# Optimization experiments

Hardware: AMD Instinct MI355X
Metric: run time of the kernel (lower is better)

The kernel has to match this reference:

```python
import jax, jax.numpy as jnp
import numpy as np

EPS = 1e-6
K_MEM, C_MEM = 512, 2048
SEQ, BATCH = 256, 16
NUM_LAYERS, NUM_HEADS, HEAD_DIM = 12, 12, 64
KV_DIM = NUM_LAYERS * NUM_HEADS * HEAD_DIM * 2  # 18432
NOISE_STD = 0.01
PINV_STEPS = 3
BEN_COHEN_INIT = -5.0


def approx_pinv(A, steps=PINV_STEPS):
    # Ben-Cohen iterative pseudoinverse. A: (B, M, N) -> (B, N, M)
    alpha = jnp.minimum(jnp.exp(jnp.float32(BEN_COHEN_INIT)), jnp.float32(5e-4))  # clamp(max=5e-4)
    P = alpha * jnp.swapaxes(A, -2, -1)
    for _ in range(steps):
        P = 2.0 * P - (P @ A) @ P  # matches bmm(bmm(P, A), P)
    return P


def setup_inputs() -> dict:
    key = jax.random.key(0)
    ks = jax.random.split(key, 6)
    lim = np.sqrt(6.0 / (C_MEM + KV_DIM))  # xavier_uniform
    return {
        "z_sequence": jax.random.normal(ks[0], (SEQ, BATCH, C_MEM), jnp.float32),
        "z_query": jax.random.normal(ks[1], (BATCH, C_MEM), jnp.float32),
        "noise": jax.random.normal(ks[2], (SEQ, BATCH, C_MEM), jnp.float32),
        "memory_mean": jax.random.normal(ks[3], (K_MEM, C_MEM), jnp.float32) * 0.02,
        "memory_logvar": jnp.zeros((K_MEM,), jnp.float32),
        "w_logvar": jnp.zeros((1,), jnp.float32),
        "W_M_weight": jax.random.uniform(ks[4], (KV_DIM, C_MEM), jnp.float32, -lim, lim),
    }


def reference(z_sequence, z_query, noise, memory_mean, memory_logvar, w_logvar, W_M_weight):
    B = z_query.shape[0]
    # ---- write ----
    prior_var = jnp.exp(memory_logvar) + EPS                     # (K,)
    prior_mean_b = jnp.broadcast_to(memory_mean, (B, K_MEM, C_MEM))
    z_noise = z_sequence + noise * NOISE_STD                     # (S, B, C)
    z_t = jnp.swapaxes(z_noise, 0, 1)                            # (B, S, C)
    M_pinv = approx_pinv(prior_mean_b)                           # (B, C, K)
    w = z_t @ M_pinv                                             # (B, S, K)
    w_pinv = approx_pinv(w)                                      # (B, K, S)
    new_memory_mean = w_pinv @ z_t                               # (B, K, C)
    # KL divergence (post_var == prior_var here)
    t1 = C_MEM * jnp.sum(prior_var / prior_var)
    t2 = jnp.sum((new_memory_mean - prior_mean_b) ** 2 / prior_var[None, :, None], axis=(-2, -1))
    t3 = -jnp.float32(C_MEM * K_MEM)
    t4 = C_MEM * jnp.sum(jnp.log(prior_var) - jnp.log(prior_var))
    dkl_M = jnp.mean(t1 + t2 + t3 + t4)
    # ---- read (deterministic addressing) ----
    M_pinv2 = approx_pinv(new_memory_mean)                       # (B, C, K)
    w_mean = jnp.einsum('bc,bck->bk', z_query, M_pinv2)          # (B, K)
    z_retrieved = jnp.einsum('bk,bkc->bc', w_mean, new_memory_mean)  # (B, C)
    Z_r_kv = z_retrieved @ W_M_weight.T                          # (B, kv_dim)
    wl = jnp.broadcast_to(w_logvar, w_mean.shape)
    dkl_w = 0.5 * jnp.sum(jnp.exp(wl) + w_mean ** 2 - 1.0 - wl)
    return z_retrieved, Z_r_kv, dkl_M, dkl_w
```

## Files before the change

### kernel.cpp

```cpp
#include <hip/hip_runtime.h>

#define ALPHA 5.0e-4f

typedef short s16x8 __attribute__((ext_vector_type(8)));
typedef unsigned short u16x8 __attribute__((ext_vector_type(8)));
typedef unsigned short u16x4 __attribute__((ext_vector_type(4)));
typedef float f32x4 __attribute__((ext_vector_type(4)));

__device__ __forceinline__ unsigned short f2bf(float f) {
    unsigned int u = __builtin_bit_cast(unsigned int, f);
    u += 0x7fffu + ((u >> 16) & 1u);
    return (unsigned short)(u >> 16);
}
__device__ __forceinline__ float bf2f(unsigned short h) {
    return __builtin_bit_cast(float, (unsigned int)h << 16);
}
__device__ __forceinline__ f32x4 mfma16(s16x8 a, s16x8 b, f32x4 c) {
    return __builtin_amdgcn_mfma_f32_16x16x32_bf16(a, b, c, 0, 0, 0);
}

template<int ROWS>
__device__ __forceinline__ void stage_kcontig(const float* __restrict__ src, int ld,
                                              unsigned short* __restrict__ lds, int tid)
{
#pragma unroll
    for (int it = 0; it < ROWS * 8 / 256; ++it) {
        const int g = tid + it * 256;
        const int row = g >> 3, s = g & 7;
        const float* p = src + (long long)row * ld + s * 8;
        const float4 x0 = *(const float4*)p;
        const float4 x1 = *(const float4*)(p + 4);
        u16x8 h;
        h[0] = f2bf(x0.x); h[1] = f2bf(x0.y); h[2] = f2bf(x0.z); h[3] = f2bf(x0.w);
        h[4] = f2bf(x1.x); h[5] = f2bf(x1.y); h[6] = f2bf(x1.z); h[7] = f2bf(x1.w);
        *(u16x8*)(lds + row * 64 + ((s ^ (row & 7)) << 3)) = h;
    }
}

template<int ROWS>
__device__ __forceinline__ void stage_kstrided(const float* __restrict__ src, int ld,
                                               unsigned short* __restrict__ lds, int tid)
{
    constexpr int KPT = ROWS * 64 / 256;
    const int m = tid % ROWS, kb = (tid / ROWS) * KPT;
#pragma unroll
    for (int j8 = 0; j8 < KPT / 8; ++j8) {
        u16x8 h;
#pragma unroll
        for (int j = 0; j < 8; ++j)
            h[j] = f2bf(src[(long long)(kb + j8 * 8 + j) * ld + m]);
        const int s = (kb >> 3) + j8;
        *(u16x8*)(lds + m * 64 + ((s ^ (m & 7)) << 3)) = h;
    }
}

template<int ROWS>
__device__ __forceinline__ void stage_kcontig_b(const unsigned short* __restrict__ src, int ld,
                                                unsigned short* __restrict__ lds, int tid)
{
#pragma unroll
    for (int it = 0; it < ROWS * 8 / 256; ++it) {
        const int g = tid + it * 256;
        const int row = g >> 3, s = g & 7;
        const u16x8 h = *(const u16x8*)(src + (long long)row * ld + s * 8);
        *(u16x8*)(lds + row * 64 + ((s ^ (row & 7)) << 3)) = h;
    }
}

template<int ROWS>
__device__ __forceinline__ void stage_kstrided_b(const unsigned short* __restrict__ src, int ld,
                                                 unsigned short* __restrict__ lds, int tid)
{
    constexpr int KPT = ROWS * 64 / 256;
    const int m = tid % ROWS, kb = (tid / ROWS) * KPT;
#pragma unroll
    for (int j8 = 0; j8 < KPT / 8; ++j8) {
        u16x8 h;
#pragma unroll
        for (int j = 0; j < 8; ++j)
            h[j] = src[(long long)(kb + j8 * 8 + j) * ld + m];
        const int s = (kb >> 3) + j8;
        *(u16x8*)(lds + m * 64 + ((s ^ (m & 7)) << 3)) = h;
    }
}

template<int BM, int BN, bool TA, bool TB>
__device__ __forceinline__
void gemm_dev_f32(int bx, int by,
                  const float* __restrict__ A, int lda,
                  const float* __restrict__ B, int ldb,
                  float* __restrict__ D, int ldd, int Kd)
{
    constexpr int TWM = BM / 2, TWN = BN / 2;
    constexpr int FM = TWM / 16, FN = TWN / 16;
    __shared__ unsigned short As[BM * 64];
    __shared__ unsigned short Bs[BN * 64];

    const int tid = threadIdx.x;
    const int lane = tid & 63, w = tid >> 6;
    const int wm = w >> 1, wn = w & 1;
    const int lrow = lane & 15, lk = lane >> 4;
    const int m0 = by * BM, n0 = bx * BN;

    f32x4 acc[FM][FN];
#pragma unroll
    for (int i = 0; i < FM; ++i)
#pragma unroll
        for (int j = 0; j < FN; ++j) acc[i][j] = (f32x4){0.f, 0.f, 0.f, 0.f};

    for (int k0 = 0; k0 < Kd; k0 += 64) {
        if (!TA) stage_kcontig<BM>(A + (long long)m0 * lda + k0, lda, As, tid);
        else     stage_kstrided<BM>(A + (long long)k0 * lda + m0, lda, As, tid);
        if (TB)  stage_kcontig<BN>(B + (long long)n0 * ldb + k0, ldb, Bs, tid);
        else     stage_kstrided<BN>(B + (long long)k0 * ldb + n0, ldb, Bs, tid);
        __syncthreads();
#pragma unroll
        for (int kk = 0; kk < 2; ++kk) {
            s16x8 ah[FM], bh[FN];
#pragma unroll
            for (int i = 0; i < FM; ++i) {
                const int row = wm * TWM + i * 16 + lrow;
                const int s = kk * 4 + lk;
                ah[i] = *(const s16x8*)(As + row * 64 + ((s ^ (row & 7)) << 3));
            }
#pragma unroll
            for (int j = 0; j < FN; ++j) {
                const int col = wn * TWN + j * 16 + lrow;
                const int s = kk * 4 + lk;
                bh[j] = *(const s16x8*)(Bs + col * 64 + ((s ^ (col & 7)) << 3));
            }
#pragma unroll
            for (int i = 0; i < FM; ++i)
#pragma unroll
                for (int j = 0; j < FN; ++j)
                    acc[i][j] = mfma16(ah[i], bh[j], acc[i][j]);
        }
        __syncthreads();
    }

#pragma unroll
    for (int i = 0; i < FM; ++i)
#pragma unroll
        for (int j = 0; j < FN; ++j) {
            const int col = n0 + wn * TWN + j * 16 + lrow;
#pragma unroll
            for (int r = 0; r < 4; ++r) {
                const int row = m0 + wm * TWM + i * 16 + lk * 4 + r;
                D[(long long)row * ldd + col] = acc[i][j][r];
            }
        }
}

__global__ __launch_bounds__(256)
void fused_prep_kernel(const float* __restrict__ zs, const float* __restrict__ no,
                       const float* __restrict__ zq, const float* __restrict__ mm,
                       unsigned short* __restrict__ ztb, float* __restrict__ q,
                       float* __restrict__ Gp)
{
    const int blk = blockIdx.x, t = threadIdx.x;
    if (blk % 9 == 8) {
        const int g = blk / 9;
        const int ky = g & 7;
        const int tile = g >> 3;
        gemm_dev_f32<64, 64, false, true>(
            tile & 7, tile >> 3,
            mm + ky * 256, 2048, mm + ky * 256, 2048,
            Gp + (long long)ky * 262144, 512, 256);
    } else {
        const int bs = blk - blk / 9;
        const int b = bs >> 8, sI = bs & 255;
        const long long in = ((long long)sI * 16 + b) * 2048 + t * 8;
        const f32x4 z0 = __builtin_nontemporal_load((const f32x4*)(zs + in));
        const f32x4 z1 = __builtin_nontemporal_load((const f32x4*)(zs + in + 4));
        const f32x4 n0 = __builtin_nontemporal_load((const f32x4*)(no + in));
        const f32x4 n1 = __builtin_nontemporal_load((const f32x4*)(no + in + 4));
        float zf[8];
#pragma unroll
        for (int j = 0; j < 4; ++j) {
            zf[j]     = fmaf(0.01f, n0[j], z0[j]);
            zf[j + 4] = fmaf(0.01f, n1[j], z1[j]);
        }
        u16x8 o;
#pragma unroll
        for (int j = 0; j < 8; ++j) o[j] = f2bf(zf[j]);
        *(u16x8*)(ztb + ((long long)bs * 2048 + t * 8)) = o;
        const float4 q0 = *(const float4*)(zq + b * 2048 + t * 8);
        const float4 q1 = *(const float4*)(zq + b * 2048 + t * 8 + 4);
        float qa = zf[0] * q0.x + zf[1] * q0.y + zf[2] * q0.z + zf[3] * q0.w
                 + zf[4] * q1.x + zf[5] * q1.y + zf[6] * q1.z + zf[7] * q1.w;
        __shared__ float red[256];
        red[t] = qa; __syncthreads();
        for (int st = 128; st > 0; st >>= 1) { if (t < st) red[t] += red[t + st]; __syncthreads(); }
        if (t == 0) q[bs] = red[0];
    }
}

__global__ __launch_bounds__(256)
void g1_reduce_zero_kernel(const float* __restrict__ Gp,
                           unsigned short* __restrict__ G1b,
                           float* __restrict__ wmean, float* __restrict__ out)
{
    const int blk = blockIdx.x, tid = threadIdx.x;
    if (blk < 256) {
        const int idx = blk * 256 + tid;
        f32x4 s = {0.f, 0.f, 0.f, 0.f};
#pragma unroll
        for (int p = 0; p < 8; ++p) {
            const f32x4 v = *(const f32x4*)(Gp + (long long)p * 262144 + idx * 4);
            s[0] += v[0]; s[1] += v[1]; s[2] += v[2]; s[3] += v[3];
        }
        u16x4 h;
#pragma unroll
        for (int j = 0; j < 4; ++j) h[j] = f2bf(s[j]);
        *(u16x4*)(G1b + idx * 4) = h;
    } else {
        const int zb = blk - 256;
        float4* oz = (float4*)(out + 32768);
        const int base = (zb * 256 + tid) * 32;
#pragma unroll
        for (int i = 0; i < 32; ++i) oz[base + i] = (float4){0.f, 0.f, 0.f, 0.f};
        if (zb == 0) {
            float4* wm4 = (float4*)wmean;
            for (int i = tid; i < 2048; i += 256) wm4[i] = (float4){0.f, 0.f, 0.f, 0.f};
            if (tid == 0) out[327680] = 0.f;
        }
    }
}

__global__ __launch_bounds__(256)
void p1_kernel(const float* __restrict__ mm, const unsigned short* __restrict__ G1b,
               unsigned short* __restrict__ P1b)
{
    constexpr int BM = 64, BN = 64, TWM = 32, TWN = 32, FM = 2, FN = 2;
    __shared__ unsigned short As[BM * 64];
    __shared__ unsigned short Bs[BN * 64];
    const int blk = blockIdx.x;
    const int bx = blk & 7, by = blk >> 3;
    const int tid = threadIdx.x;
    const int lane = tid & 63, w = tid >> 6;
    const int wm = w >> 1, wn = w & 1;
    const int lrow = lane & 15, lk = lane >> 4;
    const int m0 = by * BM, n0 = bx * BN;

    f32x4 acc[FM][FN];
#pragma unroll
    for (int i = 0; i < FM; ++i)
#pragma unroll
        for (int j = 0; j < FN; ++j) acc[i][j] = (f32x4){0.f, 0.f, 0.f, 0.f};

    for (int k0 = 0; k0 < 512; k0 += 64) {
        stage_kstrided<BM>(mm + (long long)k0 * 2048 + m0, 2048, As, tid);
        stage_kstrided_b<BN>(G1b + (long long)k0 * 512 + n0, 512, Bs, tid);
        __syncthreads();
#pragma unroll
        for (int kk = 0; kk < 2; ++kk) {
            s16x8 ah[FM], bh[FN];
#pragma unroll
            for (int i = 0; i < FM; ++i) {
                const int row = wm * TWM + i * 16 + lrow;
                const int s = kk * 4 + lk;
                ah[i] = *(const s16x8*)(As + row * 64 + ((s ^ (row & 7)) << 3));
            }
#pragma unroll
            for (int j = 0; j < FN; ++j) {
                const int col = wn * TWN + j * 16 + lrow;
                const int s = kk * 4 + lk;
                bh[j] = *(const s16x8*)(Bs + col * 64 + ((s ^ (col & 7)) << 3));
            }
#pragma unroll
            for (int i = 0; i < FM; ++i)
#pragma unroll
                for (int j = 0; j < FN; ++j)
                    acc[i][j] = mfma16(ah[i], bh[j], acc[i][j]);
        }
        __syncthreads();
    }

    const float al = -28.0f * ALPHA * ALPHA, be = 8.0f * ALPHA;
#pragma unroll
    for (int i = 0; i < FM; ++i)
#pragma unroll
        for (int j = 0; j < FN; ++j) {
            const int col = n0 + wn * TWN + j * 16 + lrow;
#pragma unroll
            for (int r = 0; r < 4; ++r) {
                const int row = m0 + wm * TWM + i * 16 + lk * 4 + r;
                const float v = fmaf(be, mm[(long long)col * 2048 + row], al * acc[i][j][r]);
                P1b[(long long)row * 512 + col] = f2bf(v);
            }
        }
}

__global__ __launch_bounds__(256)
void wT_u_kernel(const unsigned short* __restrict__ ztb,
                 const unsigned short* __restrict__ P1b,
                 unsigned short* __restrict__ wTb,
                 const float* __restrict__ q, float* __restrict__ wmean)
{
    constexpr int BM = 64, BN = 64, TWM = 32, TWN = 32, FM = 2, FN = 2;
    __shared__ unsigned short As[BM * 64];
    __shared__ unsigned short Bs[BN * 64];
    const int lin = blockIdx.x;
    const int r = lin & 7, t = lin >> 3;
    const int by = r + 8 * (t & 7), bx = t >> 3;
    const int tid = threadIdx.x;
    const int lane = tid & 63, w = tid >> 6;
    const int wm = w >> 1, wn = w & 1;
    const int lrow = lane & 15, lk = lane >> 4;
    const int m0 = by * BM, n0 = bx * BN;

    f32x4 acc[FM][FN];
#pragma unroll
    for (int i = 0; i < FM; ++i)
#pragma unroll
        for (int j = 0; j < FN; ++j) acc[i][j] = (f32x4){0.f, 0.f, 0.f, 0.f};

    for (int k0 = 0; k0 < 2048; k0 += 64) {
        stage_kcontig_b<BM>(ztb + (long long)m0 * 2048 + k0, 2048, As, tid);
        stage_kstrided_b<BN>(P1b + (long long)k0 * 512 + n0, 512, Bs, tid);
        __syncthreads();
#pragma unroll
        for (int kk = 0; kk < 2; ++kk) {
            s16x8 ah[FM], bh[FN];
#pragma unroll
            for (int i = 0; i < FM; ++i) {
                const int row = wm * TWM + i * 16 + lrow;
                const int s = kk * 4 + lk;
                ah[i] = *(const s16x8*)(As + row * 64 + ((s ^ (row & 7)) << 3));
            }
#pragma unroll
            for (int j = 0; j < FN; ++j) {
                const int col = wn * TWN + j * 16 + lrow;
                const int s = kk * 4 + lk;
                bh[j] = *(const s16x8*)(Bs + col * 64 + ((s ^ (col & 7)) << 3));
            }
#pragma unroll
            for (int i = 0; i < FM; ++i)
#pragma unroll
                for (int j = 0; j < FN; ++j)
                    acc[i][j] = mfma16(ah[i], bh[j], acc[i][j]);
        }
        __syncthreads();
    }

    float up[FN] = {0.f, 0.f};
#pragma unroll
    for (int i = 0; i < FM; ++i)
#pragma unroll
        for (int rr = 0; rr < 4; ++rr) {
            const int row = m0 + wm * TWM + i * 16 + lk * 4 + rr;
            const float qv = q[row];
#pragma unroll
            for (int j = 0; j < FN; ++j) {
                const int col = n0 + wn * TWN + j * 16 + lrow;
                const float v = acc[i][j][rr];
                wTb[(long long)(row >> 8) * 131072 + (long long)col * 256 + (row & 255)] = f2bf(v);
                up[j] = fmaf(v, qv, up[j]);
            }
        }
    const int b = m0 >> 8;
#pragma unroll
    for (int j = 0; j < FN; ++j) {
        float v = up[j];
        v += __shfl_xor(v, 16);
        v += __shfl_xor(v, 32);
        if (lk == 0) {
            const int col = n0 + wn * TWN + j * 16 + lrow;
            atomicAdd(&wmean[b * 512 + col], (64.0f * ALPHA * ALPHA) * v);
        }
    }
}

__global__ __launch_bounds__(256)
void tail1_kernel(const unsigned short* __restrict__ wTb,
                  const unsigned short* __restrict__ ztb,
                  const float* __restrict__ wmean, const float* __restrict__ wlv,
                  float* __restrict__ out)
{
    __shared__ __align__(16) float smemf[1024];
    const int blk = blockIdx.x, tid = threadIdx.x;
    if (blk < 256) {
        float* wms = smemf;
        float* ys  = smemf + 512;
        float* red2 = smemf + 768;
        const int r8 = blk & 7, t8 = blk >> 3;
        const int b = r8 + 8 * (t8 & 1), ct = t8 >> 1;
        wms[tid] = wmean[b * 512 + tid];
        wms[tid + 256] = wmean[b * 512 + 256 + tid];
        __syncthreads();
        {
            const unsigned short* wp = wTb + (long long)b * 131072 + tid;
            float yv = 0.f;
#pragma unroll 8
            for (int k = 0; k < 512; ++k)
                yv = fmaf(wms[k], bf2f(wp[(long long)k * 256]), yv);
            ys[tid] = yv;
        }
        __syncthreads();
        const int c = ct * 128 + (tid & 127), sh = tid >> 7;
        const unsigned short* zp = ztb + (long long)b * 524288 + c;
        float acc2 = 0.f;
        const int sbase = sh * 128;
#pragma unroll 8
        for (int s = 0; s < 128; ++s)
            acc2 = fmaf(ys[sbase + s], bf2f(zp[(long long)(sbase + s) * 2048]), acc2);
        red2[tid] = acc2; __syncthreads();
        if (sh == 0)
            out[(long long)b * 2048 + c] = (8.0f * ALPHA) * (red2[tid] + red2[tid + 128]);
    } else {
        float* red = smemf;
        float s = 0.f;
        for (int i = tid; i < 16 * 512; i += 256) { const float v = wmean[i]; s += v * v; }
        red[tid] = s; __syncthreads();
        for (int st = 128; st > 0; st >>= 1) { if (tid < st) red[tid] += red[tid + st]; __syncthreads(); }
        if (tid == 0) {
            const float l = wlv[0];
            out[327681] = 0.5f * (red[0] + 8192.0f * (expf(l) - 1.0f - l));
        }
    }
}

__global__ __launch_bounds__(256)
void tail2_kernel(const unsigned short* __restrict__ wTb,
                  const unsigned short* __restrict__ ztb,
                  const float* __restrict__ mm, const float* __restrict__ mlv,
                  const float* __restrict__ WM, float* __restrict__ out)
{
    __shared__ __align__(16) unsigned char smem[34304];
    const int g = blockIdx.x, tid = threadIdx.x;
    const int grp = g / 26, p = g % 26;
    if (p < 8) {
        constexpr int BM = 128, BN = 128, TWM = 64, TWN = 64, FM = 4, FN = 4;
        unsigned short* As = (unsigned short*)smem;
        unsigned short* Bs = As + BM * 64;
        float* ivars = (float*)(smem + 32768);
        float* red = (float*)(smem + 33280);
        const int bz = ((2 * grp + p) & 7) + 8 * (grp & 1);
        const int rest = grp >> 1;
        const int by = rest & 3, bx = rest >> 2;
        const int lane = tid & 63, w = tid >> 6;
        const int wm = w >> 1, wn = w & 1;
        const int lrow = lane & 15, lk = lane >> 4;
        const int m0 = by * BM, n0 = bx * BN;

        if (tid < 128) ivars[tid] = 1.0f / (expf(mlv[m0 + tid]) + 1e-6f);

        f32x4 acc[FM][FN];
#pragma unroll
        for (int i = 0; i < FM; ++i)
#pragma unroll
            for (int j = 0; j < FN; ++j) acc[i][j] = (f32x4){0.f, 0.f, 0.f, 0.f};

        for (int k0 = 0; k0 < 256; k0 += 64) {
            stage_kcontig_b<BM>(wTb + (long long)bz * 131072 + (long long)m0 * 256 + k0, 256, As, tid);
            stage_kstrided_b<BN>(ztb + (long long)bz * 524288 + (long long)k0 * 2048 + n0, 2048, Bs, tid);
            __syncthreads();
#pragma unroll
            for (int kk = 0; kk < 2; ++kk) {
                s16x8 ah[FM], bh[FN];
#pragma unroll
                for (int i = 0; i < FM; ++i) {
                    const int row = wm * TWM + i * 16 + lrow;
                    const int s = kk * 4 + lk;
                    ah[i] = *(const s16x8*)(As + row * 64 + ((s ^ (row & 7)) << 3));
                }
#pragma unroll
                for (int j = 0; j < FN; ++j) {
                    const int col = wn * TWN + j * 16 + lrow;
                    const int s = kk * 4 + lk;
                    bh[j] = *(const s16x8*)(Bs + col * 64 + ((s ^ (col & 7)) << 3));
                }
#pragma unroll
                for (int i = 0; i < FM; ++i)
#pragma unroll
                    for (int j = 0; j < FN; ++j)
                        acc[i][j] = mfma16(ah[i], bh[j], acc[i][j]);
            }
            __syncthreads();
        }

        const float A8 = 8.0f * ALPHA;
        float da = 0.f;
#pragma unroll
        for (int i = 0; i < FM; ++i)
#pragma unroll
            for (int j = 0; j < FN; ++j) {
                const int cl = wn * TWN + j * 16 + lrow;
#pragma unroll
                for (int rr = 0; rr < 4; ++rr) {
                    const int rl = wm * TWM + i * 16 + lk * 4 + rr;
                    const float v = A8 * acc[i][j][rr];
                    const float d = v - mm[(long long)(m0 + rl) * 2048 + (n0 + cl)];
                    da = fmaf(d * d, ivars[rl], da);
                }
            }
        red[tid] = da; __syncthreads();
        for (int st = 128; st > 0; st >>= 1) { if (tid < st) red[tid] += red[tid + st]; __syncthreads(); }
        if (tid == 0) atomicAdd(&out[327680], red[0] * (1.0f / 16.0f));
    } else {
        const int z = grp * 18 + (p - 8);
        const int bx = z % 288, ky = z / 288;
        const int lane = tid & 63, w = tid >> 6;
        const int d0 = bx * 64 + w * 16;
        const int kc0 = ky * 256;
        const int rr = lane & 15, kq = lane >> 4;
        const float* zr = out;
        s16x8 areg[8];
        const float* zb = zr + rr * 2048 + kc0 + kq * 8;
#pragma unroll
        for (int s = 0; s < 8; ++s) {
            const f32x4 a0 = *(const f32x4*)(zb + s * 32);
            const f32x4 a1 = *(const f32x4*)(zb + s * 32 + 4);
            u16x8 h;
#pragma unroll
            for (int j = 0; j < 4; ++j) { h[j] = f2bf(a0[j]); h[j + 4] = f2bf(a1[j]); }
            areg[s] = __builtin_bit_cast(s16x8, h);
        }
        f32x4 acc = {0.f, 0.f, 0.f, 0.f};
        const float* wb = WM + (long long)(d0 + rr) * 2048 + kc0 + kq * 8;
#pragma unroll
        for (int s = 0; s < 8; ++s) {
            const f32x4 b0 = __builtin_nontemporal_load((const f32x4*)(wb + s * 32));
            const f32x4 b1 = __builtin_nontemporal_load((const f32x4*)(wb + s * 32 + 4));
            u16x8 h;
#pragma unroll
            for (int j = 0; j < 4; ++j) { h[j] = f2bf(b0[j]); h[j + 4] = f2bf(b1[j]); }
            acc = mfma16(areg[s], __builtin_bit_cast(s16x8, h), acc);
        }
        float* oz = out + 32768;
#pragma unroll
        for (int r = 0; r < 4; ++r)
            atomicAdd(&oz[(long long)(kq * 4 + r) * 18432 + d0 + rr], acc[r]);
    }
}

extern "C" void kernel_launch(void* const* d_in, const int* in_sizes, int n_in,
                              void* d_out, int out_size, void* d_ws, size_t ws_size,
                              hipStream_t stream)
{
    (void)in_sizes; (void)n_in; (void)out_size; (void)ws_size;
    const float* z_seq   = (const float*)d_in[0];
    const float* z_query = (const float*)d_in[1];
    const float* noise   = (const float*)d_in[2];
    const float* mm      = (const float*)d_in[3];
    const float* mlv     = (const float*)d_in[4];
    const float* wlv     = (const float*)d_in[5];
    const float* WM      = (const float*)d_in[6];
    float* out = (float*)d_out;

    char* wsb = (char*)d_ws;
    unsigned short* ztb  = (unsigned short*)(wsb);
    unsigned short* wTb  = (unsigned short*)(wsb + (16LL << 20));
    float*          Gp   = (float*)(wsb + (24LL << 20));
    unsigned short* G1b  = (unsigned short*)(wsb + (32LL << 20));
    unsigned short* P1b  = (unsigned short*)(wsb + (33LL << 20));
    float*          qvec = (float*)(wsb + (36LL << 20));
    float*          wmean = (float*)(wsb + (37LL << 20));

    fused_prep_kernel<<<4608, 256, 0, stream>>>(z_seq, noise, z_query, mm,
                                                ztb, qvec, Gp);
    g1_reduce_zero_kernel<<<265, 256, 0, stream>>>(Gp, G1b, wmean, out);
    p1_kernel<<<256, 256, 0, stream>>>(mm, G1b, P1b);
    wT_u_kernel<<<512, 256, 0, stream>>>(ztb, P1b, wTb, qvec, wmean);
    tail1_kernel<<<257, 256, 0, stream>>>(wTb, ztb, wmean, wlv, out);
    tail2_kernel<<<3328, 256, 0, stream>>>(wTb, ztb, mm, mlv, WM, out);
}
```

Before: 164.0 us.

## Reassociate P1 product into Z·M^T then G1, fuse with reduce, prefetch W_M

Reorders the matrix chain: instead of forming P1 = 8αM^T - 28α²M^T G1 and then multiplying by Z (K=2048), it computes V = Z·M^T (K=2048) in the same launch as the G1 reduction. A second GEMM with K=512 then forms w = 8αV - 28α² V·G1. This drops a kernel launch and the dependency of the large GEMM on G1. Extra idle blocks in vg_kernel and tail1 read chunks of W_M so it is warm in the last-level cache for tail2, which now uses plain loads instead of nontemporal ones. The trade-offs are additional bandwidth spent on prefetch and rounding V to bf16 before the second product.

```diff
diff --git a/kernel.cpp b/kernel.cpp
--- a/kernel.cpp
+++ b/kernel.cpp
@@ -17,6 +17,19 @@
 }
 __device__ __forceinline__ f32x4 mfma16(s16x8 a, s16x8 b, f32x4 c) {
     return __builtin_amdgcn_mfma_f32_16x16x32_bf16(a, b, c, 0, 0, 0);
+}
+
+__device__ __forceinline__ void prefetch_chunk(const float* __restrict__ WM,
+                                               int chunk, int tid)
+{
+    const float4* wp = (const float4*)WM + (long long)chunk * 12288;
+    float4 s = {0.f, 0.f, 0.f, 0.f};
+#pragma unroll 8
+    for (int i = 0; i < 48; ++i) {
+        const float4 v = wp[tid + i * 256];
+        s.x += v.x; s.y += v.y; s.z += v.z; s.w += v.w;
+    }
+    asm volatile("" :: "v"(s.x), "v"(s.y), "v"(s.z), "v"(s.w));
 }
 
 template<int ROWS>
@@ -196,13 +209,70 @@
 }
 
 __global__ __launch_bounds__(256)
-void g1_reduce_zero_kernel(const float* __restrict__ Gp,
-                           unsigned short* __restrict__ G1b,
-                           float* __restrict__ wmean, float* __restrict__ out)
+void vg_kernel(const unsigned short* __restrict__ ztb, const float* __restrict__ mm,
+               const float* __restrict__ Gp, const float* __restrict__ WM,
+               unsigned short* __restrict__ Vb, unsigned short* __restrict__ G1b,
+               float* __restrict__ wmean, float* __restrict__ out)
 {
     const int blk = blockIdx.x, tid = threadIdx.x;
-    if (blk < 256) {
-        const int idx = blk * 256 + tid;
+    if (blk < 512) {
+        constexpr int BM = 64, BN = 64, TWM = 32, TWN = 32, FM = 2, FN = 2;
+        __shared__ unsigned short As[BM * 64];
+        __shared__ unsigned short Bs[BN * 64];
+        const int r = blk & 7, t = blk >> 3;
+        const int by = r + 8 * (t & 7), bx = t >> 3;
+        const int lane = tid & 63, w = tid >> 6;
+        const int wm = w >> 1, wn = w & 1;
+        const int lrow = lane & 15, lk = lane >> 4;
+        const int m0 = by * BM, n0 = bx * BN;
+
+        f32x4 acc[FM][FN];
+#pragma unroll
+        for (int i = 0; i < FM; ++i)
+#pragma unroll
+            for (int j = 0; j < FN; ++j) acc[i][j] = (f32x4){0.f, 0.f, 0.f, 0.f};
+
+        for (int k0 = 0; k0 < 2048; k0 += 64) {
+            stage_kcontig_b<BM>(ztb + (long long)m0 * 2048 + k0, 2048, As, tid);
+            stage_kcontig<BN>(mm + (long long)n0 * 2048 + k0, 2048, Bs, tid);
+            __syncthreads();
+#pragma unroll
+            for (int kk = 0; kk < 2; ++kk) {
+                s16x8 ah[FM], bh[FN];
+#pragma unroll
+                for (int i = 0; i < FM; ++i) {
+                    const int row = wm * TWM + i * 16 + lrow;
+                    const int s = kk * 4 + lk;
+                    ah[i] = *(const s16x8*)(As + row * 64 + ((s ^ (row & 7)) << 3));
+                }
+#pragma unroll
+                for (int j = 0; j < FN; ++j) {
+                    const int col = wn * TWN + j * 16 + lrow;
+                    const int s = kk * 4 + lk;
+                    bh[j] = *(const s16x8*)(Bs + col * 64 + ((s ^ (col & 7)) << 3));
+                }
+#pragma unroll
+                for (int i = 0; i < FM; ++i)
+#pragma unroll
+                    for (int j = 0; j < FN; ++j)
+                        acc[i][j] = mfma16(ah[i], bh[j], acc[i][j]);
+            }
+            __syncthreads();
+        }
+
+#pragma unroll
+        for (int i = 0; i < FM; ++i)
+#pragma unroll
+            for (int j = 0; j < FN; ++j) {
+                const int col = n0 + wn * TWN + j * 16 + lrow;
+#pragma unroll
+                for (int rr = 0; rr < 4; ++rr) {
+                    const int row = m0 + wm * TWM + i * 16 + lk * 4 + rr;
+                    Vb[(long long)row * 512 + col] = f2bf(acc[i][j][rr]);
+                }
+            }
+    } else if (blk < 768) {
+        const int idx = (blk - 512) * 256 + tid;
         f32x4 s = {0.f, 0.f, 0.f, 0.f};
 #pragma unroll
         for (int p = 0; p < 8; ++p) {
@@ -213,8 +283,8 @@
 #pragma unroll
         for (int j = 0; j < 4; ++j) h[j] = f2bf(s[j]);
         *(u16x4*)(G1b + idx * 4) = h;
-    } else {
-        const int zb = blk - 256;
+    } else if (blk < 777) {
+        const int zb = blk - 768;
         float4* oz = (float4*)(out + 32768);
         const int base = (zb * 256 + tid) * 32;
 #pragma unroll
@@ -224,78 +294,16 @@
             for (int i = tid; i < 2048; i += 256) wm4[i] = (float4){0.f, 0.f, 0.f, 0.f};
             if (tid == 0) out[327680] = 0.f;
         }
+    } else {
+        prefetch_chunk(WM, blk - 777, tid);
     }
 }
 
 __global__ __launch_bounds__(256)
-void p1_kernel(const float* __restrict__ mm, const unsigned short* __restrict__ G1b,
-               unsigned short* __restrict__ P1b)
-{
-    constexpr int BM = 64, BN = 64, TWM = 32, TWN = 32, FM = 2, FN = 2;
-    __shared__ unsigned short As[BM * 64];
-    __shared__ unsigned short Bs[BN * 64];
-    const int blk = blockIdx.x;
-    const int bx = blk & 7, by = blk >> 3;
-    const int tid = threadIdx.x;
-    const int lane = tid & 63, w = tid >> 6;
-    const int wm = w >> 1, wn = w & 1;
-    const int lrow = lane & 15, lk = lane >> 4;
-    const int m0 = by * BM, n0 = bx * BN;
-
-    f32x4 acc[FM][FN];
-#pragma unroll
-    for (int i = 0; i < FM; ++i)
-#pragma unroll
-        for (int j = 0; j < FN; ++j) acc[i][j] = (f32x4){0.f, 0.f, 0.f, 0.f};
-
-    for (int k0 = 0; k0 < 512; k0 += 64) {
-        stage_kstrided<BM>(mm + (long long)k0 * 2048 + m0, 2048, As, tid);
-        stage_kstrided_b<BN>(G1b + (long long)k0 * 512 + n0, 512, Bs, tid);
-        __syncthreads();
-#pragma unroll
-        for (int kk = 0; kk < 2; ++kk) {
-            s16x8 ah[FM], bh[FN];
-#pragma unroll
-            for (int i = 0; i < FM; ++i) {
-                const int row = wm * TWM + i * 16 + lrow;
-                const int s = kk * 4 + lk;
-                ah[i] = *(const s16x8*)(As + row * 64 + ((s ^ (row & 7)) << 3));
-            }
-#pragma unroll
-            for (int j = 0; j < FN; ++j) {
-                const int col = wn * TWN + j * 16 + lrow;
-                const int s = kk * 4 + lk;
-                bh[j] = *(const s16x8*)(Bs + col * 64 + ((s ^ (col & 7)) << 3));
-            }
-#pragma unroll
-            for (int i = 0; i < FM; ++i)
-#pragma unroll
-                for (int j = 0; j < FN; ++j)
-                    acc[i][j] = mfma16(ah[i], bh[j], acc[i][j]);
-        }
-        __syncthreads();
-    }
-
-    const float al = -28.0f * ALPHA * ALPHA, be = 8.0f * ALPHA;
-#pragma unroll
-    for (int i = 0; i < FM; ++i)
-#pragma unroll
-        for (int j = 0; j < FN; ++j) {
-            const int col = n0 + wn * TWN + j * 16 + lrow;
-#pragma unroll
-            for (int r = 0; r < 4; ++r) {
-                const int row = m0 + wm * TWM + i * 16 + lk * 4 + r;
-                const float v = fmaf(be, mm[(long long)col * 2048 + row], al * acc[i][j][r]);
-                P1b[(long long)row * 512 + col] = f2bf(v);
-            }
-        }
-}
-
-__global__ __launch_bounds__(256)
-void wT_u_kernel(const unsigned short* __restrict__ ztb,
-                 const unsigned short* __restrict__ P1b,
-                 unsigned short* __restrict__ wTb,
-                 const float* __restrict__ q, float* __restrict__ wmean)
+void wT2_kernel(const unsigned short* __restrict__ Vb,
+                const unsigned short* __restrict__ G1b,
+                unsigned short* __restrict__ wTb,
+                const float* __restrict__ q, float* __restrict__ wmean)
 {
     constexpr int BM = 64, BN = 64, TWM = 32, TWN = 32, FM = 2, FN = 2;
     __shared__ unsigned short As[BM * 64];
@@ -315,9 +323,9 @@
 #pragma unroll
         for (int j = 0; j < FN; ++j) acc[i][j] = (f32x4){0.f, 0.f, 0.f, 0.f};
 
-    for (int k0 = 0; k0 < 2048; k0 += 64) {
-        stage_kcontig_b<BM>(ztb + (long long)m0 * 2048 + k0, 2048, As, tid);
-        stage_kstrided_b<BN>(P1b + (long long)k0 * 512 + n0, 512, Bs, tid);
+    for (int k0 = 0; k0 < 512; k0 += 64) {
+        stage_kcontig_b<BM>(Vb + (long long)m0 * 512 + k0, 512, As, tid);
+        stage_kcontig_b<BN>(G1b + (long long)n0 * 512 + k0, 512, Bs, tid);
         __syncthreads();
 #pragma unroll
         for (int kk = 0; kk < 2; ++kk) {
@@ -343,6 +351,7 @@
         __syncthreads();
     }
 
+    const float a8 = 8.0f * ALPHA, a28 = -28.0f * ALPHA * ALPHA;
     float up[FN] = {0.f, 0.f};
 #pragma unroll
     for (int i = 0; i < FM; ++i)
@@ -353,7 +362,8 @@
 #pragma unroll
             for (int j = 0; j < FN; ++j) {
                 const int col = n0 + wn * TWN + j * 16 + lrow;
-                const float v = acc[i][j][rr];
+                const float v = fmaf(a8, bf2f(Vb[(long long)row * 512 + col]),
+                                     a28 * acc[i][j][rr]);
                 wTb[(long long)(row >> 8) * 131072 + (long long)col * 256 + (row & 255)] = f2bf(v);
                 up[j] = fmaf(v, qv, up[j]);
             }
@@ -375,7 +385,7 @@
 void tail1_kernel(const unsigned short* __restrict__ wTb,
                   const unsigned short* __restrict__ ztb,
                   const float* __restrict__ wmean, const float* __restrict__ wlv,
-                  float* __restrict__ out)
+                  const float* __restrict__ WM, float* __restrict__ out)
 {
     __shared__ __align__(16) float smemf[1024];
     const int blk = blockIdx.x, tid = threadIdx.x;
@@ -407,7 +417,7 @@
         red2[tid] = acc2; __syncthreads();
         if (sh == 0)
             out[(long long)b * 2048 + c] = (8.0f * ALPHA) * (red2[tid] + red2[tid + 128]);
-    } else {
+    } else if (blk == 256) {
         float* red = smemf;
         float s = 0.f;
         for (int i = tid; i < 16 * 512; i += 256) { const float v = wmean[i]; s += v * v; }
@@ -417,6 +427,8 @@
             const float l = wlv[0];
             out[327681] = 0.5f * (red[0] + 8192.0f * (expf(l) - 1.0f - l));
         }
+    } else {
+        prefetch_chunk(WM, 512 + (blk - 257), tid);
     }
 }
 
@@ -520,8 +532,8 @@
         const float* wb = WM + (long long)(d0 + rr) * 2048 + kc0 + kq * 8;
 #pragma unroll
         for (int s = 0; s < 8; ++s) {
-            const f32x4 b0 = __builtin_nontemporal_load((const f32x4*)(wb + s * 32));
-            const f32x4 b1 = __builtin_nontemporal_load((const f32x4*)(wb + s * 32 + 4));
+            const f32x4 b0 = *(const f32x4*)(wb + s * 32);
+            const f32x4 b1 = *(const f32x4*)(wb + s * 32 + 4);
             u16x8 h;
 #pragma unroll
             for (int j = 0; j < 4; ++j) { h[j] = f2bf(b0[j]); h[j + 4] = f2bf(b1[j]); }
@@ -553,15 +565,14 @@
     unsigned short* wTb  = (unsigned short*)(wsb + (16LL << 20));
     float*          Gp   = (float*)(wsb + (24LL << 20));
     unsigned short* G1b  = (unsigned short*)(wsb + (32LL << 20));
-    unsigned short* P1b  = (unsigned short*)(wsb + (33LL << 20));
-    float*          qvec = (float*)(wsb + (36LL << 20));
-    float*          wmean = (float*)(wsb + (37LL << 20));
+    unsigned short* Vb   = (unsigned short*)(wsb + (33LL << 20));
+    float*          qvec = (float*)(wsb + (38LL << 20));
+    float*          wmean = (float*)(wsb + (39LL << 20));
 
     fused_prep_kernel<<<4608, 256, 0, stream>>>(z_seq, noise, z_query, mm,
                                                 ztb, qvec, Gp);
-    g1_reduce_zero_kernel<<<265, 256, 0, stream>>>(Gp, G1b, wmean, out);
-    p1_kernel<<<256, 256, 0, stream>>>(mm, G1b, P1b);
-    wT_u_kernel<<<512, 256, 0, stream>>>(ztb, P1b, wTb, qvec, wmean);
-    tail1_kernel<<<257, 256, 0, stream>>>(wTb, ztb, wmean, wlv, out);
+    vg_kernel<<<1289, 256, 0, stream>>>(ztb, mm, Gp, WM, Vb, G1b, wmean, out);
+    wT2_kernel<<<512, 256, 0, stream>>>(Vb, G1b, wTb, qvec, wmean);
+    tail1_kernel<<<513, 256, 0, stream>>>(wTb, ztb, wmean, wlv, WM, out);
     tail2_kernel<<<3328, 256, 0, stream>>>(wTb, ztb, mm, mlv, WM, out);
 }
```

Result: faster. 160.0 us (median of 2 runs) (-2.4%).
